# Kernel tuning notes

Hardware: AMD Instinct MI355X
Metric: run time of the kernel (lower is better)

Reference implementation:

```python
import jax, jax.numpy as jnp
import numpy as np
from jax import lax

N, C, K, M = 131072, 128, 27, 65536
EPS = 1e-5


def setup_inputs() -> dict:
    key = jax.random.key(0)
    ks = jax.random.split(key, 8)
    w_scale = 1.0 / np.sqrt(K * C)  # sane fan-in init for stacked kernel weights
    return {
        "x": jax.random.normal(ks[0], (N, C), jnp.float32),
        "W1": jax.random.normal(ks[1], (K, C, C), jnp.float32) * w_scale,
        "gamma1": jnp.ones((C,), jnp.float32),
        "beta1": jnp.zeros((C,), jnp.float32),
        "W2": jax.random.normal(ks[2], (K, C, C), jnp.float32) * w_scale,
        "gamma2": jnp.ones((C,), jnp.float32),
        "beta2": jnp.zeros((C,), jnp.float32),
        "map1_in": jax.random.randint(ks[3], (K, M), 0, N, jnp.int32),
        "map1_out": jax.random.randint(ks[4], (K, M), 0, N, jnp.int32),
        "map2_in": jax.random.randint(ks[5], (K, M), 0, N, jnp.int32),
        "map2_out": jax.random.randint(ks[6], (K, M), 0, N, jnp.int32),
    }


def sparse_conv(x, W, idx_in, idx_out):
    # gather-GEMM-scatter over K kernel offsets (Minkowski kernel map)
    def body(acc, kmap):
        w, ii, io = kmap                      # [C,C], [M], [M]
        contrib = x[ii] @ w                   # gather [M,C] then GEMM
        return acc.at[io].add(contrib), None  # scatter-add
    out, _ = lax.scan(body, jnp.zeros((x.shape[0], W.shape[-1]), x.dtype),
                      (W, idx_in, idx_out))
    return out


def batch_norm(x, gamma, beta):
    m = jnp.mean(x, axis=0)
    v = jnp.var(x, axis=0)
    return (x - m) * lax.rsqrt(v + EPS) * gamma + beta


def reference(x, W1, gamma1, beta1, W2, gamma2, beta2,
              map1_in, map1_out, map2_in, map2_out):
    residual = x
    out = sparse_conv(x, W1, map1_in, map1_out)
    out = jax.nn.elu(batch_norm(out, gamma1, beta1))
    out = sparse_conv(out, W2, map2_in, map2_out)
    out = batch_norm(out, gamma2, beta2) + residual
    return jax.nn.elu(out)
```

## Files before the change

### kernel.cpp

```cpp
#include <hip/hip_runtime.h>

typedef unsigned short u16;
typedef unsigned int u32;

#define NPTS 131072
#define CD 128
#define KOFF 27
#define MMAP 65536
#define LDAB 136
#define LDC 132

__device__ __forceinline__ u16 f2bf(float f) {
  u32 u = __float_as_uint(f);
  u32 r = (u + 0x7fffu + ((u >> 16) & 1u)) >> 16;
  return (u16)r;
}

typedef __attribute__((ext_vector_type(8))) short bf16x8;
typedef __attribute__((ext_vector_type(4))) float f32x4;

__global__ __launch_bounds__(256) void k_convert_x(const float* __restrict__ x,
                                                   u16* __restrict__ xb) {
  long i = ((long)blockIdx.x * 256 + threadIdx.x) * 8;
  float4 a = *(const float4*)(x + i);
  float4 b = *(const float4*)(x + i + 4);
  uint4 v;
  v.x = f2bf(a.x) | ((u32)f2bf(a.y) << 16);
  v.y = f2bf(a.z) | ((u32)f2bf(a.w) << 16);
  v.z = f2bf(b.x) | ((u32)f2bf(b.y) << 16);
  v.w = f2bf(b.z) | ((u32)f2bf(b.w) << 16);
  *(uint4*)(xb + i) = v;
}

__global__ __launch_bounds__(256) void k_convert_w(const float* __restrict__ W,
                                                   u16* __restrict__ Wb) {
  int idx = blockIdx.x * 256 + threadIdx.x;
  if (idx >= KOFF * 2048) return;
  int k = idx >> 11;
  int rem = idx & 2047;
  int co = rem >> 4;
  int cc = rem & 15;
  const float* ws = W + (long)k * (CD * CD) + (long)(cc * 8) * CD + co;
  u16 t[8];
#pragma unroll
  for (int j = 0; j < 8; ++j) t[j] = f2bf(ws[j * CD]);
  uint4 v;
  v.x = t[0] | ((u32)t[1] << 16);
  v.y = t[2] | ((u32)t[3] << 16);
  v.z = t[4] | ((u32)t[5] << 16);
  v.w = t[6] | ((u32)t[7] << 16);
  ((uint4*)Wb)[idx] = v;
}

__global__ __launch_bounds__(256) void k_hist(const int* __restrict__ mo,
                                              u32* __restrict__ hist) {
  int i = blockIdx.x * 256 + threadIdx.x;
  atomicAdd(&hist[mo[i]], 1u);
}

__global__ __launch_bounds__(256) void k_scanA(const u32* __restrict__ hist,
                                               u32* __restrict__ offs,
                                               u32* __restrict__ bsum) {
  __shared__ u32 sh[256];
  int t = threadIdx.x, b = blockIdx.x, i = b * 256 + t;
  u32 v = hist[i];
  u32 run = v;
  sh[t] = run;
  __syncthreads();
  for (int d = 1; d < 256; d <<= 1) {
    u32 y = (t >= d) ? sh[t - d] : 0u;
    __syncthreads();
    run += y;
    sh[t] = run;
    __syncthreads();
  }
  offs[i] = run - v;
  if (t == 255) bsum[b] = run;
}

__global__ __launch_bounds__(512) void k_scanB(u32* __restrict__ bsum) {
  __shared__ u32 sh[512];
  int t = threadIdx.x;
  u32 v = bsum[t];
  u32 run = v;
  sh[t] = run;
  __syncthreads();
  for (int d = 1; d < 512; d <<= 1) {
    u32 y = (t >= d) ? sh[t - d] : 0u;
    __syncthreads();
    run += y;
    sh[t] = run;
    __syncthreads();
  }
  bsum[t] = run - v;
}

__global__ __launch_bounds__(256) void k_scanC(u32* __restrict__ offs,
                                               const u32* __restrict__ bsum, u32 cnt) {
  int t = threadIdx.x, b = blockIdx.x, i = b * 256 + t;
  offs[i] += bsum[b];
  if (i == 0) offs[NPTS] = cnt;
}

__global__ __launch_bounds__(256) void k_rank(const int* __restrict__ mo,
                                              const u32* __restrict__ offs,
                                              u32* __restrict__ cur,
                                              u32* __restrict__ rank) {
  int i = blockIdx.x * 256 + threadIdx.x;
  int o = mo[i];
  rank[i] = offs[o] + atomicAdd(&cur[o], 1u);
}

__global__ __launch_bounds__(256) void k_gemm3(const u16* __restrict__ src,
                                               const u16* __restrict__ Wb,
                                               const int* __restrict__ mi,
                                               const u32* __restrict__ rank,
                                               u16* __restrict__ contrib,
                                               int kbase) {
  __shared__ u16 As[64 * LDAB];
  __shared__ u16 Bs[128 * LDAB];
  __shared__ u32 sin[64];
  __shared__ u32 srow[64];
  const int t = threadIdx.x;
  const int b = blockIdx.x;
  const int klocal = b >> 10;
  const int i0 = klocal * MMAP + (b & 1023) * 64;

  if (t < 64) {
    sin[t] = (u32)mi[i0 + t];
    srow[t] = rank[i0 + t];
  }
  const uint4* wsrc = (const uint4*)(Wb + (long)(kbase + klocal) * (CD * CD));
#pragma unroll
  for (int i = 0; i < 8; ++i) {
    int q = i * 256 + t;
    int co = q >> 4, cc = q & 15;
    *(uint4*)&Bs[co * LDAB + cc * 8] = wsrc[q];
  }
  __syncthreads();
#pragma unroll
  for (int i = 0; i < 4; ++i) {
    int q = i * 256 + t;
    int r = q >> 4, cc = q & 15;
    long row = sin[r];
    *(uint4*)&As[r * LDAB + cc * 8] = ((const uint4*)(src + row * CD))[cc];
  }
  __syncthreads();

  const int wave = t >> 6, lane = t & 63;
  const int lr = lane & 15, quad = lane >> 4;
  const int wm = (wave & 1) * 32;
  const int wn = (wave >> 1) * 64;
  f32x4 acc[2][4] = {};
#pragma unroll
  for (int kk = 0; kk < 4; ++kk) {
    bf16x8 a[2], bfr[4];
#pragma unroll
    for (int mt = 0; mt < 2; ++mt)
      a[mt] = *(const bf16x8*)&As[(wm + mt * 16 + lr) * LDAB + (kk * 4 + quad) * 8];
#pragma unroll
    for (int nt = 0; nt < 4; ++nt)
      bfr[nt] = *(const bf16x8*)&Bs[(wn + nt * 16 + lr) * LDAB + (kk * 4 + quad) * 8];
#pragma unroll
    for (int mt = 0; mt < 2; ++mt)
#pragma unroll
      for (int nt = 0; nt < 4; ++nt)
        acc[mt][nt] = __builtin_amdgcn_mfma_f32_16x16x32_bf16(a[mt], bfr[nt], acc[mt][nt], 0, 0, 0);
  }

  __syncthreads();
  u16* Cs = As;
#pragma unroll
  for (int mt = 0; mt < 2; ++mt)
#pragma unroll
    for (int v = 0; v < 4; ++v) {
      int slot = wm + mt * 16 + quad * 4 + v;
#pragma unroll
      for (int nt = 0; nt < 4; ++nt)
        Cs[slot * LDC + wn + nt * 16 + lr] = f2bf(acc[mt][nt][v]);
    }
  __syncthreads();
#pragma unroll
  for (int i = 0; i < 4; ++i) {
    int q = i * 256 + t;
    int r = q >> 4, cc = q & 15;
    size_t rk = srow[r];
    *(uint4*)(contrib + rk * CD + cc * 8) = *(const uint4*)&Cs[r * LDC + cc * 8];
  }
}

__global__ __launch_bounds__(256) void k_segreduce3(const u16* __restrict__ contrib,
                                                    const u32* __restrict__ offs,
                                                    float* __restrict__ acc,
                                                    float* __restrict__ stats,
                                                    int first, int last) {
  const int wave = threadIdx.x >> 6, lane = threadIdx.x & 63;
  const int w = blockIdx.x * 4 + wave;
  float sx = 0.f, sx2 = 0.f, sy = 0.f, sy2 = 0.f;
  for (int row = w; row < NPTS; row += 4096) {
    u32 s0 = offs[row], s1 = offs[row + 1];
    float a0 = 0.f, b0 = 0.f, a1 = 0.f, b1 = 0.f;
    u32 e = s0;
    for (; e + 2 <= s1; e += 2) {
      u32 d0 = ((const u32*)(contrib + (size_t)e * CD))[lane];
      u32 d1 = ((const u32*)(contrib + (size_t)(e + 1) * CD))[lane];
      a0 += __uint_as_float(d0 << 16);
      b0 += __uint_as_float(d0 & 0xffff0000u);
      a1 += __uint_as_float(d1 << 16);
      b1 += __uint_as_float(d1 & 0xffff0000u);
    }
    if (e < s1) {
      u32 d0 = ((const u32*)(contrib + (size_t)e * CD))[lane];
      a0 += __uint_as_float(d0 << 16);
      b0 += __uint_as_float(d0 & 0xffff0000u);
    }
    float cx = a0 + a1, cy = b0 + b1;
    float2* ap = (float2*)(acc + (size_t)row * CD) + lane;
    if (!first) {
      float2 p = *ap;
      cx += p.x;
      cy += p.y;
    }
    *ap = make_float2(cx, cy);
    if (last) {
      sx += cx;
      sx2 += cx * cx;
      sy += cy;
      sy2 += cy * cy;
    }
  }
  if (last) {
    __shared__ float sh[1024];
    sh[threadIdx.x] = sx;
    sh[256 + threadIdx.x] = sx2;
    sh[512 + threadIdx.x] = sy;
    sh[768 + threadIdx.x] = sy2;
    __syncthreads();
    if (threadIdx.x < 64) {
      int l = threadIdx.x;
      float vx = sh[l] + sh[l + 64] + sh[l + 128] + sh[l + 192];
      float vx2 = sh[256 + l] + sh[256 + l + 64] + sh[256 + l + 128] + sh[256 + l + 192];
      float vy = sh[512 + l] + sh[512 + l + 64] + sh[512 + l + 128] + sh[512 + l + 192];
      float vy2 = sh[768 + l] + sh[768 + l + 64] + sh[768 + l + 128] + sh[768 + l + 192];
      atomicAdd(&stats[2 * l], vx);
      atomicAdd(&stats[128 + 2 * l], vx2);
      atomicAdd(&stats[2 * l + 1], vy);
      atomicAdd(&stats[128 + 2 * l + 1], vy2);
    }
  }
}

__global__ void k_finalize(const float* __restrict__ stats, const float* __restrict__ gamma,
                           const float* __restrict__ beta, float* __restrict__ scsh) {
  int c = threadIdx.x;
  float mean = stats[c] * (1.f / NPTS);
  float var = stats[128 + c] * (1.f / NPTS) - mean * mean;
  float sc = rsqrtf(var + 1e-5f) * gamma[c];
  scsh[c] = sc;
  scsh[128 + c] = beta[c] - mean * sc;
}

__device__ __forceinline__ float elu(float v) { return v > 0.f ? v : expf(v) - 1.f; }

__global__ __launch_bounds__(256) void k_apply_mid(const float* __restrict__ acc,
                                                   const float* __restrict__ scsh,
                                                   u16* __restrict__ y) {
  long i = ((long)blockIdx.x * 256 + threadIdx.x) * 4;
  int c = (int)(i & 127);
  float4 a = *(const float4*)(acc + i);
  float r0 = elu(a.x * scsh[c] + scsh[128 + c]);
  float r1 = elu(a.y * scsh[c + 1] + scsh[129 + c]);
  float r2 = elu(a.z * scsh[c + 2] + scsh[130 + c]);
  float r3 = elu(a.w * scsh[c + 3] + scsh[131 + c]);
  uint2 v;
  v.x = f2bf(r0) | ((u32)f2bf(r1) << 16);
  v.y = f2bf(r2) | ((u32)f2bf(r3) << 16);
  *(uint2*)(y + i) = v;
}

__global__ __launch_bounds__(256) void k_apply_final(const float* __restrict__ acc,
                                                     const float* __restrict__ scsh,
                                                     const float* __restrict__ x,
                                                     float* __restrict__ out) {
  long i = ((long)blockIdx.x * 256 + threadIdx.x) * 4;
  int c = (int)(i & 127);
  float4 a = *(const float4*)(acc + i);
  float4 rx = *(const float4*)(x + i);
  float4 o;
  o.x = elu(a.x * scsh[c] + scsh[128 + c] + rx.x);
  o.y = elu(a.y * scsh[c + 1] + scsh[129 + c] + rx.y);
  o.z = elu(a.z * scsh[c + 2] + scsh[130 + c] + rx.z);
  o.w = elu(a.w * scsh[c + 3] + scsh[131 + c] + rx.w);
  *(float4*)(out + i) = o;
}

extern "C" void kernel_launch(void* const* d_in, const int* in_sizes, int n_in,
                              void* d_out, int out_size, void* d_ws, size_t ws_size,
                              hipStream_t stream) {
  const float* x = (const float*)d_in[0];
  const float* W1 = (const float*)d_in[1];
  const float* g1 = (const float*)d_in[2];
  const float* b1 = (const float*)d_in[3];
  const float* W2 = (const float*)d_in[4];
  const float* g2 = (const float*)d_in[5];
  const float* b2 = (const float*)d_in[6];
  const int* m1i = (const int*)d_in[7];
  const int* m1o = (const int*)d_in[8];
  const int* m2i = (const int*)d_in[9];
  const int* m2o = (const int*)d_in[10];
  float* out = (float*)d_out;

  char* base = (char*)d_ws;
  size_t off = 0;
  auto alloc = [&](size_t bytes) -> void* {
    void* r = base + off;
    off = (off + bytes + 255) & ~(size_t)255;
    return r;
  };
  u16* xb = (u16*)alloc((size_t)NPTS * CD * 2);
  u16* yb = (u16*)alloc((size_t)NPTS * CD * 2);
  u16* Wb1 = (u16*)alloc((size_t)KOFF * CD * CD * 2);
  u16* Wb2 = (u16*)alloc((size_t)KOFF * CD * CD * 2);
  float* acc = (float*)alloc((size_t)NPTS * CD * 4);
  u32* hist = (u32*)alloc((size_t)NPTS * 4);
  u32* cur = (u32*)alloc((size_t)NPTS * 4);
  size_t msSize = (size_t)((char*)base + off - (char*)hist);
  u32* offs = (u32*)alloc(((size_t)NPTS + 1) * 4);
  float* stats = (float*)alloc(256 * 4);
  float* scsh = (float*)alloc(256 * 4);
  u32* bsum = (u32*)alloc(512 * 4);

  size_t per_k = (size_t)MMAP * CD * 2 + (size_t)MMAP * 4 + 512;
  size_t avail = (ws_size > off + 4096) ? (ws_size - off - 4096) : 0;
  int kcnt = (int)(avail / per_k);
  if (kcnt < 1) kcnt = 1;
  if (kcnt > KOFF) kcnt = KOFF;
  u32* rank = (u32*)alloc((size_t)kcnt * MMAP * 4);
  u16* contrib = (u16*)alloc((size_t)kcnt * MMAP * CD * 2);

  k_convert_x<<<(NPTS * CD) / 2048, 256, 0, stream>>>(x, xb);
  k_convert_w<<<(KOFF * 2048 + 255) / 256, 256, 0, stream>>>(W1, Wb1);
  k_convert_w<<<(KOFF * 2048 + 255) / 256, 256, 0, stream>>>(W2, Wb2);

  auto run_conv = [&](const u16* srcm, const u16* Wbm, const int* mi, const int* mo) {
    hipMemsetAsync(stats, 0, 1024, stream);
    for (int g0 = 0; g0 < KOFF; g0 += kcnt) {
      int kc = (KOFF - g0 < kcnt) ? (KOFF - g0) : kcnt;
      u32 cnt = (u32)kc * MMAP;
      hipMemsetAsync(hist, 0, msSize, stream);
      k_hist<<<cnt / 256, 256, 0, stream>>>(mo + (long)g0 * MMAP, hist);
      k_scanA<<<512, 256, 0, stream>>>(hist, offs, bsum);
      k_scanB<<<1, 512, 0, stream>>>(bsum);
      k_scanC<<<512, 256, 0, stream>>>(offs, bsum, cnt);
      k_rank<<<cnt / 256, 256, 0, stream>>>(mo + (long)g0 * MMAP, offs, cur, rank);
      k_gemm3<<<kc * 1024, 256, 0, stream>>>(srcm, Wbm, mi + (long)g0 * MMAP, rank, contrib, g0);
      k_segreduce3<<<1024, 256, 0, stream>>>(contrib, offs, acc, stats,
                                             g0 == 0 ? 1 : 0, (g0 + kc == KOFF) ? 1 : 0);
    }
  };

  run_conv(xb, Wb1, m1i, m1o);
  k_finalize<<<1, 128, 0, stream>>>(stats, g1, b1, scsh);
  k_apply_mid<<<(NPTS * CD) / 1024, 256, 0, stream>>>(acc, scsh, yb);

  run_conv(yb, Wb2, m2i, m2o);
  k_finalize<<<1, 128, 0, stream>>>(stats, g2, b2, scsh);
  k_apply_final<<<(NPTS * CD) / 1024, 256, 0, stream>>>(acc, scsh, x, out);
}
```

Before: 1.459 ms.

## Replace sort-based segmented reduction with direct fp32 atomic scatter-add

Removes the histogram/scan/rank counting-sort pipeline and the bf16 contrib buffer. The GEMM kernel now atomically adds fp32 results straight into the accumulator at the output indices, and a separate stats kernel computes the BN moments. The accumulator is zeroed by a memset and by the mid-apply kernel, and the bf16 x buffer is reused for the intermediate activations. The aim is to cut many kernel launches and the extra contrib write and read traffic. In exchange it relies on roughly 226M float atomics into a 64MB array, which could contend or run slowly.

```diff
diff --git a/kernel.cpp b/kernel.cpp
--- a/kernel.cpp
+++ b/kernel.cpp
@@ -8,7 +8,6 @@
 #define KOFF 27
 #define MMAP 65536
 #define LDAB 136
-#define LDC 132
 
 __device__ __forceinline__ u16 f2bf(float f) {
   u32 u = __float_as_uint(f);
@@ -52,71 +51,11 @@
   ((uint4*)Wb)[idx] = v;
 }
 
-__global__ __launch_bounds__(256) void k_hist(const int* __restrict__ mo,
-                                              u32* __restrict__ hist) {
-  int i = blockIdx.x * 256 + threadIdx.x;
-  atomicAdd(&hist[mo[i]], 1u);
-}
-
-__global__ __launch_bounds__(256) void k_scanA(const u32* __restrict__ hist,
-                                               u32* __restrict__ offs,
-                                               u32* __restrict__ bsum) {
-  __shared__ u32 sh[256];
-  int t = threadIdx.x, b = blockIdx.x, i = b * 256 + t;
-  u32 v = hist[i];
-  u32 run = v;
-  sh[t] = run;
-  __syncthreads();
-  for (int d = 1; d < 256; d <<= 1) {
-    u32 y = (t >= d) ? sh[t - d] : 0u;
-    __syncthreads();
-    run += y;
-    sh[t] = run;
-    __syncthreads();
-  }
-  offs[i] = run - v;
-  if (t == 255) bsum[b] = run;
-}
-
-__global__ __launch_bounds__(512) void k_scanB(u32* __restrict__ bsum) {
-  __shared__ u32 sh[512];
-  int t = threadIdx.x;
-  u32 v = bsum[t];
-  u32 run = v;
-  sh[t] = run;
-  __syncthreads();
-  for (int d = 1; d < 512; d <<= 1) {
-    u32 y = (t >= d) ? sh[t - d] : 0u;
-    __syncthreads();
-    run += y;
-    sh[t] = run;
-    __syncthreads();
-  }
-  bsum[t] = run - v;
-}
-
-__global__ __launch_bounds__(256) void k_scanC(u32* __restrict__ offs,
-                                               const u32* __restrict__ bsum, u32 cnt) {
-  int t = threadIdx.x, b = blockIdx.x, i = b * 256 + t;
-  offs[i] += bsum[b];
-  if (i == 0) offs[NPTS] = cnt;
-}
-
-__global__ __launch_bounds__(256) void k_rank(const int* __restrict__ mo,
-                                              const u32* __restrict__ offs,
-                                              u32* __restrict__ cur,
-                                              u32* __restrict__ rank) {
-  int i = blockIdx.x * 256 + threadIdx.x;
-  int o = mo[i];
-  rank[i] = offs[o] + atomicAdd(&cur[o], 1u);
-}
-
-__global__ __launch_bounds__(256) void k_gemm3(const u16* __restrict__ src,
+__global__ __launch_bounds__(256) void k_gemm4(const u16* __restrict__ src,
                                                const u16* __restrict__ Wb,
                                                const int* __restrict__ mi,
-                                               const u32* __restrict__ rank,
-                                               u16* __restrict__ contrib,
-                                               int kbase) {
+                                               const int* __restrict__ mo,
+                                               float* __restrict__ acc) {
   __shared__ u16 As[64 * LDAB];
   __shared__ u16 Bs[128 * LDAB];
   __shared__ u32 sin[64];
@@ -128,9 +67,9 @@
 
   if (t < 64) {
     sin[t] = (u32)mi[i0 + t];
-    srow[t] = rank[i0 + t];
-  }
-  const uint4* wsrc = (const uint4*)(Wb + (long)(kbase + klocal) * (CD * CD));
+    srow[t] = (u32)mo[i0 + t];
+  }
+  const uint4* wsrc = (const uint4*)(Wb + (long)klocal * (CD * CD));
 #pragma unroll
   for (int i = 0; i < 8; ++i) {
     int q = i * 256 + t;
@@ -151,7 +90,7 @@
   const int lr = lane & 15, quad = lane >> 4;
   const int wm = (wave & 1) * 32;
   const int wn = (wave >> 1) * 64;
-  f32x4 acc[2][4] = {};
+  f32x4 C[2][4] = {};
 #pragma unroll
   for (int kk = 0; kk < 4; ++kk) {
     bf16x8 a[2], bfr[4];
@@ -165,87 +104,51 @@
     for (int mt = 0; mt < 2; ++mt)
 #pragma unroll
       for (int nt = 0; nt < 4; ++nt)
-        acc[mt][nt] = __builtin_amdgcn_mfma_f32_16x16x32_bf16(a[mt], bfr[nt], acc[mt][nt], 0, 0, 0);
-  }
-
+        C[mt][nt] = __builtin_amdgcn_mfma_f32_16x16x32_bf16(a[mt], bfr[nt], C[mt][nt], 0, 0, 0);
+  }
+
+#pragma unroll
+  for (int mt = 0; mt < 2; ++mt)
+#pragma unroll
+    for (int v = 0; v < 4; ++v) {
+      int lrow = wm + mt * 16 + quad * 4 + v;
+      float* dst = acc + (size_t)srow[lrow] * CD + wn + lr;
+#pragma unroll
+      for (int nt = 0; nt < 4; ++nt)
+        atomicAdd(dst + nt * 16, C[mt][nt][v]);
+    }
+}
+
+__global__ __launch_bounds__(256) void k_stats(const float* __restrict__ acc,
+                                               float* __restrict__ stats) {
+  const int t = threadIdx.x;
+  const long total = (long)NPTS * CD / 4;
+  const long stride = (long)gridDim.x * 256;
+  long idx = (long)blockIdx.x * 256 + t;
+  float s0 = 0.f, s1 = 0.f, s2 = 0.f, s3 = 0.f;
+  float q0 = 0.f, q1 = 0.f, q2 = 0.f, q3 = 0.f;
+  for (long i = idx; i < total; i += stride) {
+    float4 a = *(const float4*)(acc + i * 4);
+    s0 += a.x; q0 += a.x * a.x;
+    s1 += a.y; q1 += a.y * a.y;
+    s2 += a.z; q2 += a.z * a.z;
+    s3 += a.w; q3 += a.w * a.w;
+  }
+  __shared__ float sh[2048];
+  sh[t * 8 + 0] = s0; sh[t * 8 + 1] = s1; sh[t * 8 + 2] = s2; sh[t * 8 + 3] = s3;
+  sh[t * 8 + 4] = q0; sh[t * 8 + 5] = q1; sh[t * 8 + 6] = q2; sh[t * 8 + 7] = q3;
   __syncthreads();
-  u16* Cs = As;
-#pragma unroll
-  for (int mt = 0; mt < 2; ++mt)
-#pragma unroll
-    for (int v = 0; v < 4; ++v) {
-      int slot = wm + mt * 16 + quad * 4 + v;
-#pragma unroll
-      for (int nt = 0; nt < 4; ++nt)
-        Cs[slot * LDC + wn + nt * 16 + lr] = f2bf(acc[mt][nt][v]);
-    }
-  __syncthreads();
-#pragma unroll
-  for (int i = 0; i < 4; ++i) {
-    int q = i * 256 + t;
-    int r = q >> 4, cc = q & 15;
-    size_t rk = srow[r];
-    *(uint4*)(contrib + rk * CD + cc * 8) = *(const uint4*)&Cs[r * LDC + cc * 8];
-  }
-}
-
-__global__ __launch_bounds__(256) void k_segreduce3(const u16* __restrict__ contrib,
-                                                    const u32* __restrict__ offs,
-                                                    float* __restrict__ acc,
-                                                    float* __restrict__ stats,
-                                                    int first, int last) {
-  const int wave = threadIdx.x >> 6, lane = threadIdx.x & 63;
-  const int w = blockIdx.x * 4 + wave;
-  float sx = 0.f, sx2 = 0.f, sy = 0.f, sy2 = 0.f;
-  for (int row = w; row < NPTS; row += 4096) {
-    u32 s0 = offs[row], s1 = offs[row + 1];
-    float a0 = 0.f, b0 = 0.f, a1 = 0.f, b1 = 0.f;
-    u32 e = s0;
-    for (; e + 2 <= s1; e += 2) {
-      u32 d0 = ((const u32*)(contrib + (size_t)e * CD))[lane];
-      u32 d1 = ((const u32*)(contrib + (size_t)(e + 1) * CD))[lane];
-      a0 += __uint_as_float(d0 << 16);
-      b0 += __uint_as_float(d0 & 0xffff0000u);
-      a1 += __uint_as_float(d1 << 16);
-      b1 += __uint_as_float(d1 & 0xffff0000u);
-    }
-    if (e < s1) {
-      u32 d0 = ((const u32*)(contrib + (size_t)e * CD))[lane];
-      a0 += __uint_as_float(d0 << 16);
-      b0 += __uint_as_float(d0 & 0xffff0000u);
-    }
-    float cx = a0 + a1, cy = b0 + b1;
-    float2* ap = (float2*)(acc + (size_t)row * CD) + lane;
-    if (!first) {
-      float2 p = *ap;
-      cx += p.x;
-      cy += p.y;
-    }
-    *ap = make_float2(cx, cy);
-    if (last) {
-      sx += cx;
-      sx2 += cx * cx;
-      sy += cy;
-      sy2 += cy * cy;
-    }
-  }
-  if (last) {
-    __shared__ float sh[1024];
-    sh[threadIdx.x] = sx;
-    sh[256 + threadIdx.x] = sx2;
-    sh[512 + threadIdx.x] = sy;
-    sh[768 + threadIdx.x] = sy2;
-    __syncthreads();
-    if (threadIdx.x < 64) {
-      int l = threadIdx.x;
-      float vx = sh[l] + sh[l + 64] + sh[l + 128] + sh[l + 192];
-      float vx2 = sh[256 + l] + sh[256 + l + 64] + sh[256 + l + 128] + sh[256 + l + 192];
-      float vy = sh[512 + l] + sh[512 + l + 64] + sh[512 + l + 128] + sh[512 + l + 192];
-      float vy2 = sh[768 + l] + sh[768 + l + 64] + sh[768 + l + 128] + sh[768 + l + 192];
-      atomicAdd(&stats[2 * l], vx);
-      atomicAdd(&stats[128 + 2 * l], vx2);
-      atomicAdd(&stats[2 * l + 1], vy);
-      atomicAdd(&stats[128 + 2 * l + 1], vy2);
+  if (t < 32) {
+#pragma unroll
+    for (int j = 0; j < 4; ++j) {
+      float a = 0.f, qq = 0.f;
+#pragma unroll
+      for (int g = 0; g < 8; ++g) {
+        a += sh[(t + g * 32) * 8 + j];
+        qq += sh[(t + g * 32) * 8 + 4 + j];
+      }
+      atomicAdd(&stats[t * 4 + j], a);
+      atomicAdd(&stats[128 + t * 4 + j], qq);
     }
   }
 }
@@ -262,7 +165,7 @@
 
 __device__ __forceinline__ float elu(float v) { return v > 0.f ? v : expf(v) - 1.f; }
 
-__global__ __launch_bounds__(256) void k_apply_mid(const float* __restrict__ acc,
+__global__ __launch_bounds__(256) void k_apply_mid(float* __restrict__ acc,
                                                    const float* __restrict__ scsh,
                                                    u16* __restrict__ y) {
   long i = ((long)blockIdx.x * 256 + threadIdx.x) * 4;
@@ -276,6 +179,7 @@
   v.x = f2bf(r0) | ((u32)f2bf(r1) << 16);
   v.y = f2bf(r2) | ((u32)f2bf(r3) << 16);
   *(uint2*)(y + i) = v;
+  *(float4*)(acc + i) = make_float4(0.f, 0.f, 0.f, 0.f);
 }
 
 __global__ __launch_bounds__(256) void k_apply_final(const float* __restrict__ acc,
@@ -318,52 +222,26 @@
     return r;
   };
   u16* xb = (u16*)alloc((size_t)NPTS * CD * 2);
-  u16* yb = (u16*)alloc((size_t)NPTS * CD * 2);
   u16* Wb1 = (u16*)alloc((size_t)KOFF * CD * CD * 2);
   u16* Wb2 = (u16*)alloc((size_t)KOFF * CD * CD * 2);
   float* acc = (float*)alloc((size_t)NPTS * CD * 4);
-  u32* hist = (u32*)alloc((size_t)NPTS * 4);
-  u32* cur = (u32*)alloc((size_t)NPTS * 4);
-  size_t msSize = (size_t)((char*)base + off - (char*)hist);
-  u32* offs = (u32*)alloc(((size_t)NPTS + 1) * 4);
   float* stats = (float*)alloc(256 * 4);
   float* scsh = (float*)alloc(256 * 4);
-  u32* bsum = (u32*)alloc(512 * 4);
-
-  size_t per_k = (size_t)MMAP * CD * 2 + (size_t)MMAP * 4 + 512;
-  size_t avail = (ws_size > off + 4096) ? (ws_size - off - 4096) : 0;
-  int kcnt = (int)(avail / per_k);
-  if (kcnt < 1) kcnt = 1;
-  if (kcnt > KOFF) kcnt = KOFF;
-  u32* rank = (u32*)alloc((size_t)kcnt * MMAP * 4);
-  u16* contrib = (u16*)alloc((size_t)kcnt * MMAP * CD * 2);
-
+
+  hipMemsetAsync(acc, 0, (size_t)NPTS * CD * 4, stream);
   k_convert_x<<<(NPTS * CD) / 2048, 256, 0, stream>>>(x, xb);
   k_convert_w<<<(KOFF * 2048 + 255) / 256, 256, 0, stream>>>(W1, Wb1);
   k_convert_w<<<(KOFF * 2048 + 255) / 256, 256, 0, stream>>>(W2, Wb2);
 
-  auto run_conv = [&](const u16* srcm, const u16* Wbm, const int* mi, const int* mo) {
-    hipMemsetAsync(stats, 0, 1024, stream);
-    for (int g0 = 0; g0 < KOFF; g0 += kcnt) {
-      int kc = (KOFF - g0 < kcnt) ? (KOFF - g0) : kcnt;
-      u32 cnt = (u32)kc * MMAP;
-      hipMemsetAsync(hist, 0, msSize, stream);
-      k_hist<<<cnt / 256, 256, 0, stream>>>(mo + (long)g0 * MMAP, hist);
-      k_scanA<<<512, 256, 0, stream>>>(hist, offs, bsum);
-      k_scanB<<<1, 512, 0, stream>>>(bsum);
-      k_scanC<<<512, 256, 0, stream>>>(offs, bsum, cnt);
-      k_rank<<<cnt / 256, 256, 0, stream>>>(mo + (long)g0 * MMAP, offs, cur, rank);
-      k_gemm3<<<kc * 1024, 256, 0, stream>>>(srcm, Wbm, mi + (long)g0 * MMAP, rank, contrib, g0);
-      k_segreduce3<<<1024, 256, 0, stream>>>(contrib, offs, acc, stats,
-                                             g0 == 0 ? 1 : 0, (g0 + kc == KOFF) ? 1 : 0);
-    }
-  };
-
-  run_conv(xb, Wb1, m1i, m1o);
+  k_gemm4<<<KOFF * 1024, 256, 0, stream>>>(xb, Wb1, m1i, m1o, acc);
+  hipMemsetAsync(stats, 0, 1024, stream);
+  k_stats<<<2048, 256, 0, stream>>>(acc, stats);
   k_finalize<<<1, 128, 0, stream>>>(stats, g1, b1, scsh);
-  k_apply_mid<<<(NPTS * CD) / 1024, 256, 0, stream>>>(acc, scsh, yb);
-
-  run_conv(yb, Wb2, m2i, m2o);
+  k_apply_mid<<<(NPTS * CD) / 1024, 256, 0, stream>>>(acc, scsh, xb);
+
+  k_gemm4<<<KOFF * 1024, 256, 0, stream>>>(xb, Wb2, m2i, m2o, acc);
+  hipMemsetAsync(stats, 0, 1024, stream);
+  k_stats<<<2048, 256, 0, stream>>>(acc, stats);
   k_finalize<<<1, 128, 0, stream>>>(stats, g2, b2, scsh);
   k_apply_final<<<(NPTS * CD) / 1024, 256, 0, stream>>>(acc, scsh, x, out);
 }
```

Result: slower. 2.028 ms (+39.0%).
